# Kernel tuning notes

Measured on AMD Instinct MI355X. Metric: run time of the kernel, lower is better.

## Reference

```python
import jax, jax.numpy as jnp
import numpy as np

D_IN = 2048
D_OUT = 2048
NUM_HEADS = 16
HEAD_DIM = D_OUT // NUM_HEADS
CONTEXT_LENGTH = 4096
THETA_BASE = 10000.0


def _rope_tables(seq_len):
    half = HEAD_DIM // 2
    inv_freq = 1.0 / (THETA_BASE ** (jnp.arange(half, dtype=jnp.float32) / half))
    positions = jnp.arange(seq_len, dtype=jnp.float32)
    angles = positions[:, None] * inv_freq[None, :]          # [S, half]
    angles = jnp.concatenate([angles, angles], axis=-1)      # [S, HEAD_DIM]
    return jnp.cos(angles), jnp.sin(angles)


def _apply_rope(x, cos, sin):
    # x: [B, H, S, D]
    half = x.shape[-1] // 2
    x1, x2 = x[..., :half], x[..., half:]
    rotated = jnp.concatenate([-x2, x1], axis=-1)
    return x * cos[None, None, :, :] + rotated * sin[None, None, :, :]


def setup_inputs() -> dict:
    key = jax.random.key(0)
    ks = jax.random.split(key, 5)
    x = jax.random.normal(ks[0], (1, 4096, D_IN), dtype=jnp.float32)
    scale_in = 1.0 / np.sqrt(D_IN)
    scale_out = 1.0 / np.sqrt(D_OUT)
    w_q = jax.random.normal(ks[1], (D_OUT, D_IN), dtype=jnp.float32) * scale_in
    w_k = jax.random.normal(ks[2], (D_OUT, D_IN), dtype=jnp.float32) * scale_in
    w_v = jax.random.normal(ks[3], (D_OUT, D_IN), dtype=jnp.float32) * scale_in
    w_o = jax.random.normal(ks[4], (D_IN, D_OUT), dtype=jnp.float32) * scale_out
    return {"x": x, "w_q": w_q, "w_k": w_k, "w_v": w_v, "w_o": w_o}


def reference(x, w_q, w_k, w_v, w_o):
    b, s, _ = x.shape
    cos, sin = _rope_tables(s)

    def split_heads(t):  # [B,S,D_OUT] -> [B,H,S,HEAD_DIM]
        return t.reshape(b, s, NUM_HEADS, HEAD_DIM).transpose(0, 2, 1, 3)

    q = split_heads(jnp.einsum('bsd,od->bso', x, w_q))
    k = split_heads(jnp.einsum('bsd,od->bso', x, w_k))
    v = split_heads(jnp.einsum('bsd,od->bso', x, w_v))

    q = _apply_rope(q, cos, sin)
    k = _apply_rope(k, cos, sin)

    scores = jnp.einsum('bhqd,bhkd->bhqk', q, k) / jnp.sqrt(jnp.float32(HEAD_DIM))
    causal = jnp.tril(jnp.ones((s, s), dtype=bool))
    scores = jnp.where(causal[None, None, :, :], scores, -jnp.inf)
    attn = jax.nn.softmax(scores, axis=-1)

    ctx = jnp.einsum('bhqk,bhkd->bhqd', attn, v)  # [B,H,S,HEAD_DIM]
    ctx = ctx.transpose(0, 2, 1, 3).reshape(b, s, D_OUT)
    return jnp.einsum('bso,do->bsd', ctx, w_o)
```

## Files before the change

### kernel.cpp

```cpp
#include <hip/hip_runtime.h>
#include <hip/hip_bf16.h>
#include <stdint.h>

#define SEQ 4096
#define DM 2048
#define NH 16
#define HD 128

typedef __attribute__((ext_vector_type(4)))  float f32x4;
typedef __attribute__((ext_vector_type(16))) float f32x16;
typedef __attribute__((ext_vector_type(8)))  short bf16x8;
typedef __attribute__((ext_vector_type(4)))  float float4_t;
typedef __attribute__((ext_vector_type(4)))  short s16x4;
typedef __attribute__((ext_vector_type(2)))  int   i32x2;
typedef __attribute__((ext_vector_type(2)))  unsigned u32x2;

__device__ __forceinline__ short f2bf(float f) {
  union { float f; unsigned u; } c; c.f = f;
  unsigned u = c.u;
  u += 0x7FFFu + ((u >> 16) & 1u);
  return (short)(u >> 16);
}

__device__ __forceinline__ int cvtpk(float lo, float hi) {
  int r;
  asm("v_cvt_pk_bf16_f32 %0, %1, %2" : "=v"(r) : "v"(lo), "v"(hi));
  return r;
}

__device__ __forceinline__ float exp2r(float x) {
  return __builtin_amdgcn_exp2f(x);
}

__device__ __forceinline__ void async16(const void* g, void* l) {
  __builtin_amdgcn_global_load_lds((const __attribute__((address_space(1))) void*)g,
                                   (__attribute__((address_space(3))) void*)l, 16, 0, 0);
}

__global__ __launch_bounds__(256) void rope_tables_kernel(float2* __restrict__ tab) {
  int idx = blockIdx.x * 256 + threadIdx.x;
  int s = idx >> 6, j = idx & 63;
  float invf = expf(-(float)j * (9.210340371976184f / 64.0f));
  float ang = (float)s * invf;
  tab[idx] = make_float2(cosf(ang), sinf(ang));
}

__global__ __launch_bounds__(256) void f32_to_bf16_kernel(const float* __restrict__ in,
                                                          short* __restrict__ out, int n4) {
  int stride = gridDim.x * 256;
  for (int i = blockIdx.x * 256 + threadIdx.x; i < n4; i += stride) {
    float4_t v = ((const float4_t*)in)[i];
    s16x4 r;
    #pragma unroll
    for (int u = 0; u < 4; u++) r[u] = f2bf(v[u]);
    ((s16x4*)out)[i] = r;
  }
}

template<int OUT_MODE>
__global__ __launch_bounds__(256) void gemm_async_kernel(
    const short* __restrict__ A, const short* __restrict__ B,
    void* __restrict__ Cp, int M, int N, int K) {
  __shared__ short As[128 * 64];
  __shared__ short Bs[128 * 64];
  const int t = threadIdx.x, lane = t & 63, w = t >> 6;
  const int wr = w >> 1, wc = w & 1;
  const size_t Mbase = (size_t)blockIdx.x * 128;
  const size_t Nbase = (size_t)blockIdx.y * 128;
  f32x4 acc[4][4] = {};

  for (int k0 = 0; k0 < K; k0 += 64) {
    __syncthreads();
    #pragma unroll
    for (int c = 0; c < 4; c++) {
      int ob = w * 4096 + c * 1024;
      int o = ob + lane * 16;
      int row = o >> 7;
      int cb = (o & 127) ^ ((row & 7) << 4);
      async16((const char*)A + ((Mbase + row) * (size_t)K + k0) * 2 + cb, (char*)As + ob);
      async16((const char*)B + ((Nbase + row) * (size_t)K + k0) * 2 + cb, (char*)Bs + ob);
    }
    __syncthreads();

    bf16x8 a[2][4], b[2][4];
    #pragma unroll
    for (int ks = 0; ks < 2; ks++) {
      #pragma unroll
      for (int m = 0; m < 4; m++) {
        int row = wr * 64 + m * 16 + (lane & 15);
        int chunk = ks * 64 + (lane >> 4) * 16;
        a[ks][m] = *(const bf16x8*)((const char*)As + row * 128 + (chunk ^ ((row & 7) << 4)));
      }
      #pragma unroll
      for (int n = 0; n < 4; n++) {
        int row = wc * 64 + n * 16 + (lane & 15);
        int chunk = ks * 64 + (lane >> 4) * 16;
        b[ks][n] = *(const bf16x8*)((const char*)Bs + row * 128 + (chunk ^ ((row & 7) << 4)));
      }
    }
    #pragma unroll
    for (int ks = 0; ks < 2; ks++)
      #pragma unroll
      for (int m = 0; m < 4; m++)
        #pragma unroll
        for (int n = 0; n < 4; n++)
          acc[m][n] = __builtin_amdgcn_mfma_f32_16x16x32_bf16(a[ks][m], b[ks][n], acc[m][n], 0, 0, 0);
  }

  #pragma unroll
  for (int m = 0; m < 4; m++)
    #pragma unroll
    for (int n = 0; n < 4; n++)
      #pragma unroll
      for (int j = 0; j < 4; j++) {
        size_t row = Mbase + wr * 64 + m * 16 + (lane >> 4) * 4 + j;
        size_t col = Nbase + wc * 64 + n * 16 + (lane & 15);
        float v = acc[m][n][j];
        if (OUT_MODE == 0) ((float*)Cp)[row * N + col] = v;
        else               ((short*)Cp)[col * (size_t)M + row] = f2bf(v);
      }
}

template<int IS_Q>
__global__ __launch_bounds__(256) void gemm_rope_kernel(
    const short* __restrict__ A, const short* __restrict__ B,
    short* __restrict__ C, const float2* __restrict__ tab) {
  __shared__ short As[128 * 64];
  __shared__ short Bs[128 * 64];
  const int t = threadIdx.x, lane = t & 63, w = t >> 6;
  const size_t Mbase = (size_t)blockIdx.x * 128;
  const size_t Nbase = (size_t)blockIdx.y * 128;
  const int K = DM;
  f32x4 acc[2][8] = {};

  for (int k0 = 0; k0 < K; k0 += 64) {
    __syncthreads();
    #pragma unroll
    for (int c = 0; c < 4; c++) {
      int ob = w * 4096 + c * 1024;
      int o = ob + lane * 16;
      int row = o >> 7;
      int cb = (o & 127) ^ ((row & 7) << 4);
      async16((const char*)A + ((Mbase + row) * (size_t)K + k0) * 2 + cb, (char*)As + ob);
      async16((const char*)B + ((Nbase + row) * (size_t)K + k0) * 2 + cb, (char*)Bs + ob);
    }
    __syncthreads();

    bf16x8 a[2][2], b[2][8];
    #pragma unroll
    for (int ks = 0; ks < 2; ks++) {
      #pragma unroll
      for (int m = 0; m < 2; m++) {
        int row = w * 32 + m * 16 + (lane & 15);
        int chunk = ks * 64 + (lane >> 4) * 16;
        a[ks][m] = *(const bf16x8*)((const char*)As + row * 128 + (chunk ^ ((row & 7) << 4)));
      }
      #pragma unroll
      for (int n = 0; n < 8; n++) {
        int row = n * 16 + (lane & 15);
        int chunk = ks * 64 + (lane >> 4) * 16;
        b[ks][n] = *(const bf16x8*)((const char*)Bs + row * 128 + (chunk ^ ((row & 7) << 4)));
      }
    }
    #pragma unroll
    for (int ks = 0; ks < 2; ks++)
      #pragma unroll
      for (int m = 0; m < 2; m++)
        #pragma unroll
        for (int n = 0; n < 8; n++)
          acc[m][n] = __builtin_amdgcn_mfma_f32_16x16x32_bf16(a[ks][m], b[ks][n], acc[m][n], 0, 0, 0);
  }

  const float SC = IS_Q ? 0.12751746f : 1.0f;
  #pragma unroll
  for (int m = 0; m < 2; m++)
    #pragma unroll
    for (int n = 0; n < 4; n++)
      #pragma unroll
      for (int j = 0; j < 4; j++) {
        int row = (int)Mbase + w * 32 + m * 16 + (lane >> 4) * 4 + j;
        int dj = n * 16 + (lane & 15);
        float2 cs = tab[row * 64 + dj];
        float cc = cs.x * SC, ss = cs.y * SC;
        float r1 = acc[m][n][j], r2 = acc[m][n + 4][j];
        C[(size_t)row * DM + Nbase + dj]      = f2bf(r1 * cc - r2 * ss);
        C[(size_t)row * DM + Nbase + dj + 64] = f2bf(r2 * cc + r1 * ss);
      }
}

__global__ __launch_bounds__(512) void flash_attn9_kernel(
    const short* __restrict__ Q, const short* __restrict__ K,
    const short* __restrict__ VT, short* __restrict__ O) {
  __shared__ __align__(16) char LB[65536];
  const int t = threadIdx.x, lane = t & 63, w = t >> 6;
  const int hi = lane >> 5, c31 = lane & 31;
  const int s = w & 3, v = w >> 2;
  const int id = blockIdx.x;
  const int h  = (id & 7) * 2 + ((id >> 3) & 1);
  const int pr = (id >> 4) & 15;
  const int qt = (id < 256) ? pr : (31 - pr);

  auto stage = [&](int kt, int buf) {
    #pragma unroll
    for (int it = 0; it < 2; it++) {
      const int ob = it * 8192 + w * 1024;
      const int o  = ob + lane * 16;
      const int row = o >> 8;
      const int xs = (o & 255) ^ ((row & 15) << 4);
      {
        const size_t src = ((size_t)(kt * 64 + row) * DM + h * HD) * 2 + xs;
        async16((const char*)K + src, LB + buf * 16384 + ob); }
      {
        const int d = 2 * row + (xs >> 7);
        const size_t src = ((size_t)(h * HD + d) * SEQ + (size_t)kt * 64) * 2
                         + (size_t)(xs & 127);
        async16((const char*)VT + src, LB + 32768 + buf * 16384 + ob); }
    }
  };

  const int q0 = qt * 128;
  const int nt = 2 * (qt + 1);
  const int qrow = q0 + s * 32 + c31;

  stage(0, 0);

  bf16x8 qf[8];
  #pragma unroll
  for (int ss = 0; ss < 8; ss++)
    qf[ss] = *(const bf16x8*)(Q + (size_t)qrow * DM + h * HD + ss * 16 + hi * 8);

  f32x16 oacc[4] = {};
  float m = -3.0e38f, l = 0.f;

  __syncthreads();

  for (int kt = 0; kt < nt; kt++) {
    const int buf = kt & 1;
    if (kt + 1 < nt) stage(kt + 1, buf ^ 1);

    if (kt * 64 + v * 32 <= q0 + s * 32 + 31) {
      const char* KsB = LB + buf * 16384;
      const char* VsB = LB + 32768 + buf * 16384;

      f32x16 sacc = {};
      __builtin_amdgcn_s_setprio(1);
      #pragma unroll
      for (int ss = 0; ss < 8; ss++) {
        int row = v * 32 + c31;
        bf16x8 kf = *(const bf16x8*)(KsB + row * 256
                                     + ((ss * 32 + hi * 16) ^ ((row & 15) << 4)));
        sacc = __builtin_amdgcn_mfma_f32_32x32x16_bf16(kf, qf[ss], sacc, 0, 0, 0);
      }
      __builtin_amdgcn_s_setprio(0);

      float t0[8];
      #pragma unroll
      for (int r = 0; r < 8; r++) t0[r] = fmaxf(sacc[r], sacc[r + 8]);
      #pragma unroll
      for (int d = 4; d > 0; d >>= 1)
        #pragma unroll
        for (int r = 0; r < 4; r++) if (r < d) t0[r] = fmaxf(t0[r], t0[r + d]);
      float mx = t0[0];
      i32x2 mm = __builtin_amdgcn_permlane32_swap(__float_as_int(mx), __float_as_int(mx),
                                                  false, false);
      mx = fmaxf(__int_as_float(mm.x), __int_as_float(mm.y));

      if (__any(mx > m + 11.5416f)) {
        float mn = fmaxf(m, mx);
        float al = exp2r(m - mn);
        m = mn; l *= al;
        #pragma unroll
        for (int g = 0; g < 4; g++)
          #pragma unroll
          for (int r = 0; r < 16; r++) oacc[g][r] *= al;
      }

      const int rel = qrow - kt * 64 - v * 32;
      const bool maskT = (kt * 64 + v * 32 + 31) > (q0 + s * 32);
      #pragma unroll
      for (int r = 0; r < 16; r++) {
        float e = exp2r(sacc[r] - m);
        if (maskT) {
          int kl = (r & 3) + 8 * (r >> 2) + 4 * hi;
          e = (kl > rel) ? 0.f : e;
        }
        sacc[r] = e;
      }

      float s0[8];
      #pragma unroll
      for (int r = 0; r < 8; r++) s0[r] = sacc[r] + sacc[r + 8];
      #pragma unroll
      for (int d = 4; d > 0; d >>= 1)
        #pragma unroll
        for (int r = 0; r < 4; r++) if (r < d) s0[r] = s0[r] + s0[r + d];
      l += s0[0];

      bf16x8 pa[2];
      #pragma unroll
      for (int sg = 0; sg < 2; sg++) {
        int q0a = cvtpk(sacc[8 * sg + 0], sacc[8 * sg + 1]);
        int q1a = cvtpk(sacc[8 * sg + 2], sacc[8 * sg + 3]);
        int q0b = cvtpk(sacc[8 * sg + 4], sacc[8 * sg + 5]);
        int q1b = cvtpk(sacc[8 * sg + 6], sacc[8 * sg + 7]);
        i32x2 r0 = __builtin_amdgcn_permlane32_swap(q0a, q0b, false, false);
        i32x2 r1 = __builtin_amdgcn_permlane32_swap(q1a, q1b, false, false);
        union { int d[4]; bf16x8 vv; } u;
        u.d[0] = r0.x; u.d[1] = r1.x; u.d[2] = r0.y; u.d[3] = r1.y;
        pa[sg] = u.vv;
      }

      __builtin_amdgcn_s_setprio(1);
      #pragma unroll
      for (int ks = 0; ks < 2; ks++)
        #pragma unroll
        for (int g = 0; g < 4; g++) {
          int d = g * 32 + c31;
          int row = d >> 1;
          int x = (d & 1) * 128 + v * 64 + ks * 32 + hi * 16;
          bf16x8 vf = *(const bf16x8*)(VsB + row * 256 + (x ^ ((row & 15) << 4)));
          oacc[g] = __builtin_amdgcn_mfma_f32_32x32x16_bf16(vf, pa[ks], oacc[g], 0, 0, 0);
        }
      __builtin_amdgcn_s_setprio(0);
    }
    __syncthreads();
  }

  i32x2 lr = __builtin_amdgcn_permlane32_swap(__float_as_int(l), __float_as_int(l),
                                              false, false);
  l = __int_as_float(lr.x) + __int_as_float(lr.y);

  #pragma unroll
  for (int round = 0; round < 2; round++) {
    const int reg = s & 1;
    const bool active = (s >> 1) == round;
    if (active && v == 1) {
      float* Op = (float*)(LB + reg * 16384);
      #pragma unroll
      for (int g = 0; g < 4; g++)
        #pragma unroll
        for (int rr = 0; rr < 16; rr++) {
          int d = g * 32 + (rr & 3) + 8 * (rr >> 2) + 4 * hi;
          Op[d * 32 + c31] = oacc[g][rr];
        }
      if (hi == 0) {
        float* mm2 = (float*)(LB + 32768 + reg * 256) + c31 * 2;
        mm2[0] = m; mm2[1] = l;
      }
    }
    __syncthreads();
    if (active && v == 0) {
      const float* mm2 = (const float*)(LB + 32768 + reg * 256) + c31 * 2;
      float lB = mm2[1];
      float mB = (lB > 0.f) ? mm2[0] : -3.0e38f;
      float ms = fmaxf(m, mB);
      float aA = exp2r(m - ms), aB = exp2r(mB - ms);
      float linv = 1.0f / (l * aA + lB * aB);
      float sA = aA * linv, sB = aB * linv;
      const float* Op = (const float*)(LB + reg * 16384);
      #pragma unroll
      for (int g = 0; g < 4; g++)
        #pragma unroll
        for (int tt = 0; tt < 4; tt++) {
          float o[4];
          #pragma unroll
          for (int e = 0; e < 4; e++) {
            int d = g * 32 + e + 8 * tt + 4 * hi;
            o[e] = oacc[g][4 * tt + e] * sA + Op[d * 32 + c31] * sB;
          }
          u32x2 pk;
          pk.x = (unsigned)cvtpk(o[0], o[1]);
          pk.y = (unsigned)cvtpk(o[2], o[3]);
          *(u32x2*)(O + (size_t)qrow * DM + h * HD + g * 32 + tt * 8 + hi * 4) = pk;
        }
    }
    __syncthreads();
  }
}

extern "C" void kernel_launch(void* const* d_in, const int* in_sizes, int n_in,
                              void* d_out, int out_size, void* d_ws, size_t ws_size,
                              hipStream_t stream) {
  const float* x  = (const float*)d_in[0];
  const float* wq = (const float*)d_in[1];
  const float* wk = (const float*)d_in[2];
  const float* wv = (const float*)d_in[3];
  const float* wo = (const float*)d_in[4];
  float* out = (float*)d_out;

  const size_t SQDMs = (size_t)SEQ * DM;
  short* Qb   = (short*)d_ws;
  short* Kb   = Qb + SQDMs;
  short* VTb  = Kb + SQDMs;
  short* Cb   = VTb + SQDMs;
  short* xbf  = Cb + SQDMs;
  short* wbuf = xbf + SQDMs;
  float2* tab = (float2*)(wbuf + (size_t)DM * DM);

  rope_tables_kernel<<<SEQ * 64 / 256, 256, 0, stream>>>(tab);
  f32_to_bf16_kernel<<<2048, 256, 0, stream>>>(x, xbf, (int)(SQDMs / 4));

  dim3 g(SEQ / 128, DM / 128);
  f32_to_bf16_kernel<<<2048, 256, 0, stream>>>(wq, wbuf, DM * DM / 4);
  gemm_rope_kernel<1><<<g, 256, 0, stream>>>(xbf, wbuf, Qb, tab);
  f32_to_bf16_kernel<<<2048, 256, 0, stream>>>(wk, wbuf, DM * DM / 4);
  gemm_rope_kernel<0><<<g, 256, 0, stream>>>(xbf, wbuf, Kb, tab);
  f32_to_bf16_kernel<<<2048, 256, 0, stream>>>(wv, wbuf, DM * DM / 4);
  gemm_async_kernel<2><<<g, 256, 0, stream>>>(xbf, wbuf, VTb, SEQ, DM, DM);

  flash_attn9_kernel<<<512, 512, 0, stream>>>(Qb, Kb, VTb, Cb);

  f32_to_bf16_kernel<<<2048, 256, 0, stream>>>(wo, wbuf, DM * DM / 4);
  gemm_async_kernel<0><<<g, 256, 0, stream>>>(Cb, wbuf, out, SEQ, DM, DM);
}
```

Before: 301.4 us.

## Shrink flash attention blocks to 64 query rows with single-buffered LDS

The attention kernel now uses 256-thread blocks covering 64 query rows, launched as 1024 blocks ordered longest-first, and drops K/V double buffering so LDS use falls from 64KB to about 33KB. The smaller footprint lets more blocks share a CU and gives finer-grained causal load balancing. The cost is that loads are no longer overlapped with compute: each tile is staged between two barriers, and K/V tiles are re-read from global memory for twice as many query blocks.

New measurement: 312.4 us. +3.7%, slower.

```diff
diff --git a/kernel.cpp b/kernel.cpp
--- a/kernel.cpp
+++ b/kernel.cpp
@@ -188,41 +188,37 @@
       }
 }
 
-__global__ __launch_bounds__(512) void flash_attn9_kernel(
+__global__ __launch_bounds__(256) void flash_attn12_kernel(
     const short* __restrict__ Q, const short* __restrict__ K,
     const short* __restrict__ VT, short* __restrict__ O) {
-  __shared__ __align__(16) char LB[65536];
+  __shared__ __align__(16) char LB[33280];
   const int t = threadIdx.x, lane = t & 63, w = t >> 6;
   const int hi = lane >> 5, c31 = lane & 31;
-  const int s = w & 3, v = w >> 2;
+  const int s = w & 1, v = w >> 1;
   const int id = blockIdx.x;
   const int h  = (id & 7) * 2 + ((id >> 3) & 1);
-  const int pr = (id >> 4) & 15;
-  const int qt = (id < 256) ? pr : (31 - pr);
-
-  auto stage = [&](int kt, int buf) {
-    #pragma unroll
-    for (int it = 0; it < 2; it++) {
-      const int ob = it * 8192 + w * 1024;
+  const int qt = 63 - (id >> 4);
+  const int q0 = qt * 64;
+  const int nt = qt + 1;
+  const int qrow = q0 + s * 32 + c31;
+
+  auto stage = [&](int kt) {
+    #pragma unroll
+    for (int it = 0; it < 4; it++) {
+      const int ob = w * 4096 + it * 1024;
       const int o  = ob + lane * 16;
       const int row = o >> 8;
       const int xs = (o & 255) ^ ((row & 15) << 4);
       {
         const size_t src = ((size_t)(kt * 64 + row) * DM + h * HD) * 2 + xs;
-        async16((const char*)K + src, LB + buf * 16384 + ob); }
+        async16((const char*)K + src, LB + ob); }
       {
         const int d = 2 * row + (xs >> 7);
         const size_t src = ((size_t)(h * HD + d) * SEQ + (size_t)kt * 64) * 2
                          + (size_t)(xs & 127);
-        async16((const char*)VT + src, LB + 32768 + buf * 16384 + ob); }
+        async16((const char*)VT + src, LB + 16384 + ob); }
     }
   };
-
-  const int q0 = qt * 128;
-  const int nt = 2 * (qt + 1);
-  const int qrow = q0 + s * 32 + c31;
-
-  stage(0, 0);
 
   bf16x8 qf[8];
   #pragma unroll
@@ -232,15 +228,14 @@
   f32x16 oacc[4] = {};
   float m = -3.0e38f, l = 0.f;
 
-  __syncthreads();
-
   for (int kt = 0; kt < nt; kt++) {
-    const int buf = kt & 1;
-    if (kt + 1 < nt) stage(kt + 1, buf ^ 1);
+    __syncthreads();
+    stage(kt);
+    __syncthreads();
 
     if (kt * 64 + v * 32 <= q0 + s * 32 + 31) {
-      const char* KsB = LB + buf * 16384;
-      const char* VsB = LB + 32768 + buf * 16384;
+      const char* KsB = LB;
+      const char* VsB = LB + 16384;
 
       f32x16 sacc = {};
       __builtin_amdgcn_s_setprio(1);
@@ -323,58 +318,52 @@
         }
       __builtin_amdgcn_s_setprio(0);
     }
-    __syncthreads();
-  }
+  }
+  __syncthreads();
 
   i32x2 lr = __builtin_amdgcn_permlane32_swap(__float_as_int(l), __float_as_int(l),
                                               false, false);
   l = __int_as_float(lr.x) + __int_as_float(lr.y);
 
-  #pragma unroll
-  for (int round = 0; round < 2; round++) {
-    const int reg = s & 1;
-    const bool active = (s >> 1) == round;
-    if (active && v == 1) {
-      float* Op = (float*)(LB + reg * 16384);
-      #pragma unroll
-      for (int g = 0; g < 4; g++)
-        #pragma unroll
-        for (int rr = 0; rr < 16; rr++) {
-          int d = g * 32 + (rr & 3) + 8 * (rr >> 2) + 4 * hi;
-          Op[d * 32 + c31] = oacc[g][rr];
+  if (v == 1) {
+    float* Op = (float*)(LB + s * 16384);
+    #pragma unroll
+    for (int g = 0; g < 4; g++)
+      #pragma unroll
+      for (int rr = 0; rr < 16; rr++) {
+        int d = g * 32 + (rr & 3) + 8 * (rr >> 2) + 4 * hi;
+        Op[d * 32 + c31] = oacc[g][rr];
+      }
+    if (hi == 0) {
+      float* mm2 = (float*)(LB + 32768 + s * 256) + c31 * 2;
+      mm2[0] = m; mm2[1] = l;
+    }
+  }
+  __syncthreads();
+  if (v == 0) {
+    const float* mm2 = (const float*)(LB + 32768 + s * 256) + c31 * 2;
+    float lB = mm2[1];
+    float mB = (lB > 0.f) ? mm2[0] : -3.0e38f;
+    float ms = fmaxf(m, mB);
+    float aA = exp2r(m - ms), aB = exp2r(mB - ms);
+    float linv = 1.0f / (l * aA + lB * aB);
+    float sA = aA * linv, sB = aB * linv;
+    const float* Op = (const float*)(LB + s * 16384);
+    #pragma unroll
+    for (int g = 0; g < 4; g++)
+      #pragma unroll
+      for (int tt = 0; tt < 4; tt++) {
+        float o[4];
+        #pragma unroll
+        for (int e = 0; e < 4; e++) {
+          int d = g * 32 + e + 8 * tt + 4 * hi;
+          o[e] = oacc[g][4 * tt + e] * sA + Op[d * 32 + c31] * sB;
         }
-      if (hi == 0) {
-        float* mm2 = (float*)(LB + 32768 + reg * 256) + c31 * 2;
-        mm2[0] = m; mm2[1] = l;
-      }
-    }
-    __syncthreads();
-    if (active && v == 0) {
-      const float* mm2 = (const float*)(LB + 32768 + reg * 256) + c31 * 2;
-      float lB = mm2[1];
-      float mB = (lB > 0.f) ? mm2[0] : -3.0e38f;
-      float ms = fmaxf(m, mB);
-      float aA = exp2r(m - ms), aB = exp2r(mB - ms);
-      float linv = 1.0f / (l * aA + lB * aB);
-      float sA = aA * linv, sB = aB * linv;
-      const float* Op = (const float*)(LB + reg * 16384);
-      #pragma unroll
-      for (int g = 0; g < 4; g++)
-        #pragma unroll
-        for (int tt = 0; tt < 4; tt++) {
-          float o[4];
-          #pragma unroll
-          for (int e = 0; e < 4; e++) {
-            int d = g * 32 + e + 8 * tt + 4 * hi;
-            o[e] = oacc[g][4 * tt + e] * sA + Op[d * 32 + c31] * sB;
-          }
-          u32x2 pk;
-          pk.x = (unsigned)cvtpk(o[0], o[1]);
-          pk.y = (unsigned)cvtpk(o[2], o[3]);
-          *(u32x2*)(O + (size_t)qrow * DM + h * HD + g * 32 + tt * 8 + hi * 4) = pk;
-        }
-    }
-    __syncthreads();
+        u32x2 pk;
+        pk.x = (unsigned)cvtpk(o[0], o[1]);
+        pk.y = (unsigned)cvtpk(o[2], o[3]);
+        *(u32x2*)(O + (size_t)qrow * DM + h * HD + g * 32 + tt * 8 + hi * 4) = pk;
+      }
   }
 }
 
@@ -408,7 +397,7 @@
   f32_to_bf16_kernel<<<2048, 256, 0, stream>>>(wv, wbuf, DM * DM / 4);
   gemm_async_kernel<2><<<g, 256, 0, stream>>>(xbf, wbuf, VTb, SEQ, DM, DM);
 
-  flash_attn9_kernel<<<512, 512, 0, stream>>>(Qb, Kb, VTb, Cb);
+  flash_attn12_kernel<<<1024, 256, 0, stream>>>(Qb, Kb, VTb, Cb);
 
   f32_to_bf16_kernel<<<2048, 256, 0, stream>>>(wo, wbuf, DM * DM / 4);
   gemm_async_kernel<0><<<g, 256, 0, stream>>>(Cb, wbuf, out, SEQ, DM, DM);
```

## Replace projection GEMMs with triple-buffered 256x128 eight-wave pipelined GEMM

Applied to the files above, without the earlier changes.

Replaces the three projection GEMM variants and the output GEMM with one templated kernel. It uses 512 threads, 256x128 tiles and a 3-stage async LDS ring, with prefetch two k-tiles ahead interleaved with MFMA phases, plus s_setprio and barriers. The aim is to hide global-load latency, which the old single-buffered loop exposed through two syncthreads per k step, and to raise reuse of B per block. In exchange it uses 144KB of LDS, so only one block fits per CU, and the grid is halved to 256 blocks, which can leave the wave count short of the CU count.

New measurement: 283.5 us. 1.06x faster.

```diff
diff --git a/kernel.cpp b/kernel.cpp
--- a/kernel.cpp
+++ b/kernel.cpp
@@ -57,135 +57,127 @@
   }
 }
 
-template<int OUT_MODE>
-__global__ __launch_bounds__(256) void gemm_async_kernel(
+template<int MODE>
+__global__ __launch_bounds__(512) void gemm8p_kernel(
     const short* __restrict__ A, const short* __restrict__ B,
-    void* __restrict__ Cp, int M, int N, int K) {
-  __shared__ short As[128 * 64];
-  __shared__ short Bs[128 * 64];
+    void* __restrict__ Cp, const float2* __restrict__ tab) {
+  constexpr int MM = SEQ, NN = DM, K = DM;
+  __shared__ __align__(16) char LB[147456];
   const int t = threadIdx.x, lane = t & 63, w = t >> 6;
-  const int wr = w >> 1, wc = w & 1;
-  const size_t Mbase = (size_t)blockIdx.x * 128;
+  const size_t Mbase = (size_t)blockIdx.x * 256;
   const size_t Nbase = (size_t)blockIdx.y * 128;
-  f32x4 acc[4][4] = {};
-
-  for (int k0 = 0; k0 < K; k0 += 64) {
-    __syncthreads();
-    #pragma unroll
-    for (int c = 0; c < 4; c++) {
-      int ob = w * 4096 + c * 1024;
-      int o = ob + lane * 16;
-      int row = o >> 7;
-      int cb = (o & 127) ^ ((row & 7) << 4);
-      async16((const char*)A + ((Mbase + row) * (size_t)K + k0) * 2 + cb, (char*)As + ob);
-      async16((const char*)B + ((Nbase + row) * (size_t)K + k0) * 2 + cb, (char*)Bs + ob);
-    }
-    __syncthreads();
-
-    bf16x8 a[2][4], b[2][4];
-    #pragma unroll
-    for (int ks = 0; ks < 2; ks++) {
-      #pragma unroll
-      for (int m = 0; m < 4; m++) {
-        int row = wr * 64 + m * 16 + (lane & 15);
-        int chunk = ks * 64 + (lane >> 4) * 16;
-        a[ks][m] = *(const bf16x8*)((const char*)As + row * 128 + (chunk ^ ((row & 7) << 4)));
-      }
-      #pragma unroll
-      for (int n = 0; n < 4; n++) {
-        int row = wc * 64 + n * 16 + (lane & 15);
-        int chunk = ks * 64 + (lane >> 4) * 16;
-        b[ks][n] = *(const bf16x8*)((const char*)Bs + row * 128 + (chunk ^ ((row & 7) << 4)));
-      }
-    }
-    #pragma unroll
-    for (int ks = 0; ks < 2; ks++)
-      #pragma unroll
-      for (int m = 0; m < 4; m++)
-        #pragma unroll
-        for (int n = 0; n < 4; n++)
-          acc[m][n] = __builtin_amdgcn_mfma_f32_16x16x32_bf16(a[ks][m], b[ks][n], acc[m][n], 0, 0, 0);
+  const int nt = K / 64;
+
+  auto stageA = [&](int kt, int half) {
+    const int buf = kt % 3, k0 = kt * 64;
+    #pragma unroll
+    for (int it = 0; it < 2; it++) {
+      const int ob = half * 16384 + it * 8192 + w * 1024;
+      const int o = ob + lane * 16;
+      const int row = o >> 7;
+      const int col = (o & 127) ^ ((row & 7) << 4);
+      async16((const char*)A + ((Mbase + row) * (size_t)K + k0) * 2 + col,
+              LB + buf * 32768 + ob);
+    }
+  };
+  auto stageB = [&](int kt) {
+    const int buf = kt % 3, k0 = kt * 64;
+    #pragma unroll
+    for (int it = 0; it < 2; it++) {
+      const int ob = it * 8192 + w * 1024;
+      const int o = ob + lane * 16;
+      const int row = o >> 7;
+      const int col = (o & 127) ^ ((row & 7) << 4);
+      async16((const char*)B + ((Nbase + row) * (size_t)K + k0) * 2 + col,
+              LB + 98304 + buf * 16384 + ob);
+    }
+  };
+
+  f32x4 acc[2][8] = {};
+
+  stageA(0, 0); stageA(0, 1); stageB(0);
+  stageA(1, 0); stageA(1, 1); stageB(1);
+  asm volatile("s_waitcnt vmcnt(6)" ::: "memory");
+  __builtin_amdgcn_s_barrier();
+
+  for (int kt = 0; kt < nt; kt++) {
+    const char* AsB = LB + (kt % 3) * 32768;
+    const char* BsB = LB + 98304 + (kt % 3) * 16384;
+    const bool pre = (kt + 2 < nt);
+    bf16x8 a[2][2];
+    #pragma unroll
+    for (int p = 0; p < 4; p++) {
+      bf16x8 bb[2][2];
+      if (p == 0) {
+        #pragma unroll
+        for (int ks = 0; ks < 2; ks++)
+          #pragma unroll
+          for (int m = 0; m < 2; m++) {
+            int row = w * 32 + m * 16 + (lane & 15);
+            a[ks][m] = *(const bf16x8*)(AsB + row * 128
+                        + ((ks * 64 + (lane >> 4) * 16) ^ ((row & 7) << 4)));
+          }
+      }
+      #pragma unroll
+      for (int ks = 0; ks < 2; ks++)
+        #pragma unroll
+        for (int j = 0; j < 2; j++) {
+          int row = (2 * p + j) * 16 + (lane & 15);
+          bb[ks][j] = *(const bf16x8*)(BsB + row * 128
+                       + ((ks * 64 + (lane >> 4) * 16) ^ ((row & 7) << 4)));
+        }
+      if (p == 0 && pre) stageA(kt + 2, 0);
+      if (p == 1 && pre) stageA(kt + 2, 1);
+      if (p == 2 && pre) stageB(kt + 2);
+      if (p == 3) asm volatile("s_waitcnt vmcnt(6)" ::: "memory");
+      __builtin_amdgcn_s_barrier();
+      asm volatile("s_waitcnt lgkmcnt(0)" ::: "memory");
+      __builtin_amdgcn_sched_barrier(0);
+      __builtin_amdgcn_s_setprio(1);
+      #pragma unroll
+      for (int ks = 0; ks < 2; ks++)
+        #pragma unroll
+        for (int m = 0; m < 2; m++)
+          #pragma unroll
+          for (int j = 0; j < 2; j++)
+            acc[m][2 * p + j] = __builtin_amdgcn_mfma_f32_16x16x32_bf16(
+                a[ks][m], bb[ks][j], acc[m][2 * p + j], 0, 0, 0);
+      __builtin_amdgcn_s_setprio(0);
+      __builtin_amdgcn_s_barrier();
+    }
   }
 
-  #pragma unroll
-  for (int m = 0; m < 4; m++)
-    #pragma unroll
-    for (int n = 0; n < 4; n++)
-      #pragma unroll
-      for (int j = 0; j < 4; j++) {
-        size_t row = Mbase + wr * 64 + m * 16 + (lane >> 4) * 4 + j;
-        size_t col = Nbase + wc * 64 + n * 16 + (lane & 15);
-        float v = acc[m][n][j];
-        if (OUT_MODE == 0) ((float*)Cp)[row * N + col] = v;
-        else               ((short*)Cp)[col * (size_t)M + row] = f2bf(v);
-      }
-}
-
-template<int IS_Q>
-__global__ __launch_bounds__(256) void gemm_rope_kernel(
-    const short* __restrict__ A, const short* __restrict__ B,
-    short* __restrict__ C, const float2* __restrict__ tab) {
-  __shared__ short As[128 * 64];
-  __shared__ short Bs[128 * 64];
-  const int t = threadIdx.x, lane = t & 63, w = t >> 6;
-  const size_t Mbase = (size_t)blockIdx.x * 128;
-  const size_t Nbase = (size_t)blockIdx.y * 128;
-  const int K = DM;
-  f32x4 acc[2][8] = {};
-
-  for (int k0 = 0; k0 < K; k0 += 64) {
-    __syncthreads();
-    #pragma unroll
-    for (int c = 0; c < 4; c++) {
-      int ob = w * 4096 + c * 1024;
-      int o = ob + lane * 16;
-      int row = o >> 7;
-      int cb = (o & 127) ^ ((row & 7) << 4);
-      async16((const char*)A + ((Mbase + row) * (size_t)K + k0) * 2 + cb, (char*)As + ob);
-      async16((const char*)B + ((Nbase + row) * (size_t)K + k0) * 2 + cb, (char*)Bs + ob);
-    }
-    __syncthreads();
-
-    bf16x8 a[2][2], b[2][8];
-    #pragma unroll
-    for (int ks = 0; ks < 2; ks++) {
-      #pragma unroll
-      for (int m = 0; m < 2; m++) {
-        int row = w * 32 + m * 16 + (lane & 15);
-        int chunk = ks * 64 + (lane >> 4) * 16;
-        a[ks][m] = *(const bf16x8*)((const char*)As + row * 128 + (chunk ^ ((row & 7) << 4)));
-      }
-      #pragma unroll
-      for (int n = 0; n < 8; n++) {
-        int row = n * 16 + (lane & 15);
-        int chunk = ks * 64 + (lane >> 4) * 16;
-        b[ks][n] = *(const bf16x8*)((const char*)Bs + row * 128 + (chunk ^ ((row & 7) << 4)));
-      }
-    }
-    #pragma unroll
-    for (int ks = 0; ks < 2; ks++)
-      #pragma unroll
-      for (int m = 0; m < 2; m++)
-        #pragma unroll
-        for (int n = 0; n < 8; n++)
-          acc[m][n] = __builtin_amdgcn_mfma_f32_16x16x32_bf16(a[ks][m], b[ks][n], acc[m][n], 0, 0, 0);
+  if (MODE == 1 || MODE == 2) {
+    const float SC = (MODE == 1) ? 0.12751746f : 1.0f;
+    #pragma unroll
+    for (int m = 0; m < 2; m++)
+      #pragma unroll
+      for (int n = 0; n < 4; n++)
+        #pragma unroll
+        for (int j = 0; j < 4; j++) {
+          int row = (int)Mbase + w * 32 + m * 16 + (lane >> 4) * 4 + j;
+          int dj = n * 16 + (lane & 15);
+          float2 cs = tab[row * 64 + dj];
+          float cc = cs.x * SC, ss = cs.y * SC;
+          float r1 = acc[m][n][j], r2 = acc[m][n + 4][j];
+          short* C = (short*)Cp;
+          C[(size_t)row * NN + Nbase + dj]      = f2bf(r1 * cc - r2 * ss);
+          C[(size_t)row * NN + Nbase + dj + 64] = f2bf(r2 * cc + r1 * ss);
+        }
+  } else {
+    #pragma unroll
+    for (int m = 0; m < 2; m++)
+      #pragma unroll
+      for (int n = 0; n < 8; n++)
+        #pragma unroll
+        for (int j = 0; j < 4; j++) {
+          size_t row = Mbase + w * 32 + m * 16 + (lane >> 4) * 4 + j;
+          size_t col = Nbase + n * 16 + (lane & 15);
+          float v = acc[m][n][j];
+          if (MODE == 0) ((float*)Cp)[row * NN + col] = v;
+          else           ((short*)Cp)[col * (size_t)MM + row] = f2bf(v);
+        }
   }
-
-  const float SC = IS_Q ? 0.12751746f : 1.0f;
-  #pragma unroll
-  for (int m = 0; m < 2; m++)
-    #pragma unroll
-    for (int n = 0; n < 4; n++)
-      #pragma unroll
-      for (int j = 0; j < 4; j++) {
-        int row = (int)Mbase + w * 32 + m * 16 + (lane >> 4) * 4 + j;
-        int dj = n * 16 + (lane & 15);
-        float2 cs = tab[row * 64 + dj];
-        float cc = cs.x * SC, ss = cs.y * SC;
-        float r1 = acc[m][n][j], r2 = acc[m][n + 4][j];
-        C[(size_t)row * DM + Nbase + dj]      = f2bf(r1 * cc - r2 * ss);
-        C[(size_t)row * DM + Nbase + dj + 64] = f2bf(r2 * cc + r1 * ss);
-      }
 }
 
 __global__ __launch_bounds__(512) void flash_attn9_kernel(
@@ -207,11 +199,9 @@
       const int o  = ob + lane * 16;
       const int row = o >> 8;
       const int xs = (o & 255) ^ ((row & 15) << 4);
-      {
-        const size_t src = ((size_t)(kt * 64 + row) * DM + h * HD) * 2 + xs;
+      { const size_t src = ((size_t)(kt * 64 + row) * DM + h * HD) * 2 + xs;
         async16((const char*)K + src, LB + buf * 16384 + ob); }
-      {
-        const int d = 2 * row + (xs >> 7);
+      { const int d = 2 * row + (xs >> 7);
         const size_t src = ((size_t)(h * HD + d) * SEQ + (size_t)kt * 64) * 2
                          + (size_t)(xs & 127);
         async16((const char*)VT + src, LB + 32768 + buf * 16384 + ob); }
@@ -400,16 +390,16 @@
   rope_tables_kernel<<<SEQ * 64 / 256, 256, 0, stream>>>(tab);
   f32_to_bf16_kernel<<<2048, 256, 0, stream>>>(x, xbf, (int)(SQDMs / 4));
 
-  dim3 g(SEQ / 128, DM / 128);
+  dim3 g8(SEQ / 256, DM / 128);
   f32_to_bf16_kernel<<<2048, 256, 0, stream>>>(wq, wbuf, DM * DM / 4);
-  gemm_rope_kernel<1><<<g, 256, 0, stream>>>(xbf, wbuf, Qb, tab);
+  gemm8p_kernel<1><<<g8, 512, 0, stream>>>(xbf, wbuf, Qb, tab);
   f32_to_bf16_kernel<<<2048, 256, 0, stream>>>(wk, wbuf, DM * DM / 4);
-  gemm_rope_kernel<0><<<g, 256, 0, stream>>>(xbf, wbuf, Kb, tab);
+  gemm8p_kernel<2><<<g8, 512, 0, stream>>>(xbf, wbuf, Kb, tab);
   f32_to_bf16_kernel<<<2048, 256, 0, stream>>>(wv, wbuf, DM * DM / 4);
-  gemm_async_kernel<2><<<g, 256, 0, stream>>>(xbf, wbuf, VTb, SEQ, DM, DM);
+  gemm8p_kernel<3><<<g8, 512, 0, stream>>>(xbf, wbuf, VTb, nullptr);
 
   flash_attn9_kernel<<<512, 512, 0, stream>>>(Qb, Kb, VTb, Cb);
 
   f32_to_bf16_kernel<<<2048, 256, 0, stream>>>(wo, wbuf, DM * DM / 4);
-  gemm_async_kernel<0><<<g, 256, 0, stream>>>(Cb, wbuf, out, SEQ, DM, DM);
-}
+  gemm8p_kernel<0><<<g8, 512, 0, stream>>>(Cb, wbuf, out, nullptr);
+}
```
